# Performance work log

Measured on AMD Instinct MI355X. Metric: run time of the kernel, lower is better.

The kernel has to match this reference:

```python
import jax, jax.numpy as jnp
import numpy as np

T, B, F = 160, 640, 40          # time-major input [T, B, F]
H, PJ, L = 768, 256, 3          # nb_hidden, nb_proj, nb_layers
FORGET_BIAS = 1.0               # TF LSTMCell default


def _glorot(k, shape):
    std = (2.0 / (shape[0] + shape[1])) ** 0.5
    return jax.random.normal(k, shape, jnp.float32) * std


def setup_inputs() -> dict:
    key = jax.random.key(0)
    ks = jax.random.split(key, 7)
    x = jax.random.normal(ks[0], (T, B, F), jnp.float32)
    # layer 0: input dim F + proj state PJ; layers 1,2: input dim PJ + PJ
    W0 = _glorot(ks[1], (F + PJ, 4 * H)); b0 = jnp.zeros((4 * H,), jnp.float32)
    P0 = _glorot(ks[2], (H, PJ))
    W1 = _glorot(ks[3], (PJ + PJ, 4 * H)); b1 = jnp.zeros((4 * H,), jnp.float32)
    P1 = _glorot(ks[4], (H, PJ))
    W2 = _glorot(ks[5], (PJ + PJ, 4 * H)); b2 = jnp.zeros((4 * H,), jnp.float32)
    P2 = _glorot(ks[6], (H, PJ))
    return {"x": x, "W0": W0, "b0": b0, "P0": P0,
            "W1": W1, "b1": b1, "P1": P1,
            "W2": W2, "b2": b2, "P2": P2}


def _cell(xt, c, h, W, b, P):
    # TF LSTMCell with num_proj: gates on [x, m_prev]; gate order i, j, f, o.
    z = jnp.concatenate([xt, h], axis=-1) @ W + b            # [B, 4H]
    i, j, f, o = jnp.split(z, 4, axis=-1)
    c_new = jax.nn.sigmoid(f + FORGET_BIAS) * c + jax.nn.sigmoid(i) * jnp.tanh(j)
    m = jax.nn.sigmoid(o) * jnp.tanh(c_new)                  # [B, H]
    h_new = m @ P                                            # projected state [B, PJ]
    return c_new, h_new


def reference(x, W0, b0, P0, W1, b1, P1, W2, b2, P2):
    params = ((W0, b0, P0), (W1, b1, P1), (W2, b2, P2))
    Bd = x.shape[1]
    init = tuple((jnp.zeros((Bd, H), x.dtype), jnp.zeros((Bd, PJ), x.dtype))
                 for _ in range(L))

    def step(carry, xt):
        inp = xt
        new = []
        for (c, h), (W, b, P) in zip(carry, params):
            c, h = _cell(inp, c, h, W, b, P)
            new.append((c, h))
            inp = h
        return tuple(new), None

    carry, _ = jax.lax.scan(step, init, x)
    emb = carry[-1][1]                                       # last layer h at final step, [B, PJ]
    # tf.nn.l2_normalize
    return emb / jnp.sqrt(jnp.maximum(jnp.sum(emb * emb, axis=-1, keepdims=True), 1e-12))
```

## Files before the change

kernel.cpp:

```cpp
#include <hip/hip_runtime.h>

#define Bdim 640
#define Hdim 768
#define PJdim 256
#define Tdim 160
#define NSTEP (Tdim + 2)
#define ZS 258

typedef _Float16 half8 __attribute__((ext_vector_type(8)));
typedef float floatx4 __attribute__((ext_vector_type(4)));

constexpr size_t HB_HALFS = 3ull * Bdim * PJdim;
constexpr size_t ZP_OFF   = HB_HALFS * 2;
constexpr size_t MB_OFF   = ZP_OFF + 256;
constexpr size_t MB_HALFS = 3ull * Bdim * Hdim;
constexpr size_t X_OFF    = MB_OFF + MB_HALFS * 2;
constexpr size_t X_HALFS  = (size_t)Tdim * Bdim * 40;
constexpr size_t W_OFF    = X_OFF + X_HALFS * 2;
constexpr size_t W_HALFS  = 36ull * 131072;
constexpr size_t P_OFF    = W_OFF + W_HALFS * 2;
constexpr size_t P_HALFS  = 3ull * 196608;
constexpr size_t C_OFF    = P_OFF + P_HALFS * 2;
constexpr size_t C_BYTES  = 3ull * Bdim * Hdim * 4;

__device__ __forceinline__ float sigm(float v) { return 1.0f / (1.0f + __expf(-v)); }
__device__ __forceinline__ float tanh_fast(float v) { return 2.0f / (1.0f + __expf(-2.0f * v)) - 1.0f; }

__device__ __forceinline__ uint4 ld_coh16(const void* p) {
    const unsigned long long* q = (const unsigned long long*)p;
    unsigned long long a = __hip_atomic_load(q,     __ATOMIC_RELAXED, __HIP_MEMORY_SCOPE_AGENT);
    unsigned long long b = __hip_atomic_load(q + 1, __ATOMIC_RELAXED, __HIP_MEMORY_SCOPE_AGENT);
    uint4 r; r.x = (unsigned)a; r.y = (unsigned)(a >> 32);
    r.z = (unsigned)b; r.w = (unsigned)(b >> 32);
    return r;
}
__device__ __forceinline__ void st_coh16b(void* p, _Float16 h) {
    union { _Float16 h; unsigned short u; } cv; cv.h = h;
    __hip_atomic_store((unsigned short*)p, cv.u, __ATOMIC_RELAXED, __HIP_MEMORY_SCOPE_AGENT);
}

__device__ __forceinline__ void wait1(unsigned* c, unsigned tgt)
{
    if (threadIdx.x == 0) {
        while (__hip_atomic_load(c, __ATOMIC_RELAXED, __HIP_MEMORY_SCOPE_AGENT) < tgt)
            __builtin_amdgcn_s_sleep(1);
    }
    asm volatile("buffer_inv sc0" ::: "memory");
    __syncthreads();
}

__device__ __forceinline__ void wait2(unsigned* a, unsigned* b, unsigned tgt)
{
    if (threadIdx.x == 0) {
        while (__hip_atomic_load(a, __ATOMIC_RELAXED, __HIP_MEMORY_SCOPE_AGENT) < tgt)
            __builtin_amdgcn_s_sleep(1);
        while (__hip_atomic_load(b, __ATOMIC_RELAXED, __HIP_MEMORY_SCOPE_AGENT) < tgt)
            __builtin_amdgcn_s_sleep(1);
    }
    asm volatile("buffer_inv sc0" ::: "memory");
    __syncthreads();
}

__device__ __forceinline__ void pipe_sig(unsigned* c)
{
    __syncthreads();
    if (threadIdx.x == 0)
        __hip_atomic_fetch_add(c, 1u, __ATOMIC_RELAXED, __HIP_MEMORY_SCOPE_AGENT);
}

__device__ __forceinline__ void pipe_sig2(unsigned* a, unsigned* b)
{
    __syncthreads();
    if (threadIdx.x == 0) {
        __hip_atomic_fetch_add(a, 1u, __ATOMIC_RELAXED, __HIP_MEMORY_SCOPE_AGENT);
        __hip_atomic_fetch_add(b, 1u, __ATOMIC_RELAXED, __HIP_MEMORY_SCOPE_AGENT);
    }
}

__global__ void repack_kernel(const float* __restrict__ x,
                              const float* __restrict__ W0, const float* __restrict__ W1,
                              const float* __restrict__ W2, const float* __restrict__ P0,
                              const float* __restrict__ P1, const float* __restrict__ P2,
                              _Float16* __restrict__ Wfrag, _Float16* __restrict__ Pfrag,
                              _Float16* __restrict__ x16)
{
    size_t idx = (size_t)blockIdx.x * 256 + threadIdx.x;
    if (idx < W_HALFS) {
        int slab = (int)(idx >> 17);
        int l = slab / 12, ht = slab % 12;
        int r  = (int)(idx & 131071);
        int kc = r >> 13;
        int r2 = r & 8191;
        int g  = r2 >> 11;
        int cf = (r2 >> 9) & 3;
        int u  = r2 & 511;
        int lane = u >> 3, e = u & 7;
        int qd = lane >> 4, ln = lane & 15;
        int k   = kc * 32 + qd * 8 + e;
        int col = g * Hdim + ht * 64 + cf * 16 + ln;
        float v;
        if (l == 0)      v = (k < 296) ? W0[(size_t)k * 3072 + col] : 0.0f;
        else if (l == 1) v = W1[(size_t)k * 3072 + col];
        else             v = W2[(size_t)k * 3072 + col];
        Wfrag[idx] = (_Float16)v;
    } else if (idx < W_HALFS + P_HALFS) {
        size_t i = idx - W_HALFS;
        int l = (int)(i / 196608);
        int r = (int)(i % 196608);
        int cq = r / 49152;
        int r2 = r % 49152;
        int kc = r2 / 2048;
        int r3 = r2 & 2047;
        int cgr = r3 >> 9;
        int u  = r3 & 511;
        int lane = u >> 3, e = u & 7;
        int qd = lane >> 4, ln = lane & 15;
        int k  = kc * 32 + qd * 8 + e;
        int pj = cq * 64 + cgr * 16 + ln;
        const float* P = (l == 0) ? P0 : (l == 1) ? P1 : P2;
        Pfrag[i] = (_Float16)P[(size_t)k * PJdim + pj];
    } else if (idx < W_HALFS + P_HALFS + X_HALFS) {
        size_t i = idx - W_HALFS - P_HALFS;
        x16[i] = (_Float16)x[i];
    }
}

__device__ __forceinline__ void gate_step(
    int l, int b0r, int h0, int t, bool xl,
    const half8 (&Breg)[16][2], float (&c)[16],
    const _Float16* __restrict__ x16, const _Float16* __restrict__ h16,
    const _Float16* __restrict__ zerop, _Float16* __restrict__ mbuf,
    _Float16* __restrict__ Ast, float* __restrict__ zst, const float* __restrict__ bst,
    unsigned* pd, unsigned pdt, unsigned* pdlo, unsigned pdlot, int tid)
{
    const int wv = tid >> 6, lane = tid & 63, qd = lane >> 4, ln = lane & 15;
    const int g = wv >> 1, hh = wv & 1;
    const int qd8 = qd * 8;
    const int rowg = b0r + wv * 16 + ln;

    const _Float16* xt  = x16 + ((size_t)t * Bdim + rowg) * 40;
    const _Float16* h0b = h16 + (size_t)rowg * PJdim - 40;
    const _Float16* lob = (l > 0) ? h16 + ((size_t)(l - 1) * Bdim + rowg) * PJdim : nullptr;
    const _Float16* hib = h16 + ((size_t)l * Bdim + rowg) * PJdim - 256;

    auto srcp = [&](int kc) -> const _Float16* {
        int k = kc * 32 + qd8;
        if (l == 0) return (k < 40) ? xt + k : (k < 296) ? h0b + k : zerop;
        return (k < 256) ? lob + k : hib + k;
    };

    floatx4 acc[8][2];
    const floatx4 fz = {0.f, 0.f, 0.f, 0.f};
#pragma unroll
    for (int i = 0; i < 8; ++i) { acc[i][0] = fz; acc[i][1] = fz; }

    _Float16* Aw = Ast + wv * 512 + lane * 8;

    auto stage_gemm = [&](int kc0, int nkc, bool coh) {
        const int ncp = nkc >> 1;
        uint4 p0 = coh ? ld_coh16(srcp(kc0))     : *(const uint4*)srcp(kc0);
        uint4 p1 = coh ? ld_coh16(srcp(kc0 + 1)) : *(const uint4*)srcp(kc0 + 1);
#pragma unroll
        for (int cp = 0; cp < 5; ++cp) {
            if (cp < ncp) {
                const int s0 = (cp & 1) * 2;
                *(uint4*)(Aw + (size_t)s0 * 4096)       = p0;
                *(uint4*)(Aw + (size_t)(s0 + 1) * 4096) = p1;
                if (cp + 1 < ncp) {
                    p0 = coh ? ld_coh16(srcp(kc0 + 2 * cp + 2)) : *(const uint4*)srcp(kc0 + 2 * cp + 2);
                    p1 = coh ? ld_coh16(srcp(kc0 + 2 * cp + 3)) : *(const uint4*)srcp(kc0 + 2 * cp + 3);
                }
                __syncthreads();
#pragma unroll
                for (int j = 0; j < 2; ++j) {
                    const _Float16* Ab = Ast + (size_t)(s0 + j) * 4096;
                    const int kc = kc0 + 2 * cp + j;
#pragma unroll
                    for (int rf = 0; rf < 8; ++rf) {
                        half8 af = *(const half8*)(Ab + rf * 512 + lane * 8);
                        acc[rf][0] = __builtin_amdgcn_mfma_f32_16x16x32_f16(af, Breg[kc][0], acc[rf][0], 0, 0, 0);
                        acc[rf][1] = __builtin_amdgcn_mfma_f32_16x16x32_f16(af, Breg[kc][1], acc[rf][1], 0, 0, 0);
                    }
                }
            }
        }
    };

    if (pd) wait1(pd, pdt);
    if (l == 0) {
        stage_gemm(0, 10, false);
    } else {
        stage_gemm(8, 8, false);
        if (pdlo) wait1(pdlo, pdlot);
        stage_gemm(0, 8, xl);
    }
    __syncthreads();

#pragma unroll
    for (int rf = 0; rf < 8; ++rf)
#pragma unroll
        for (int cf = 0; cf < 2; ++cf)
#pragma unroll
            for (int r = 0; r < 4; ++r)
                zst[(size_t)(rf * 16 + qd * 4 + r) * ZS + g * 64 + hh * 32 + cf * 16 + ln]
                    = acc[rf][cf][r];
    __syncthreads();

    const int row = tid >> 2, c0 = (tid & 3) * 16;
    const float* zrow = zst + (size_t)row * ZS;
    union { _Float16 h[16]; uint4 v[2]; } pk;
#pragma unroll
    for (int q = 0; q < 4; ++q) {
        const int o = q * 4;
        float4 zi = *(const float4*)(zrow + c0 + o);
        float4 zj = *(const float4*)(zrow + 64 + c0 + o);
        float4 zf = *(const float4*)(zrow + 128 + c0 + o);
        float4 zo = *(const float4*)(zrow + 192 + c0 + o);
        float4 bi = *(const float4*)(bst + c0 + o);
        float4 bj = *(const float4*)(bst + 64 + c0 + o);
        float4 bf = *(const float4*)(bst + 128 + c0 + o);
        float4 bo = *(const float4*)(bst + 192 + c0 + o);
        float cn0 = sigm(zf.x + bf.x) * c[o + 0] + sigm(zi.x + bi.x) * tanh_fast(zj.x + bj.x);
        float cn1 = sigm(zf.y + bf.y) * c[o + 1] + sigm(zi.y + bi.y) * tanh_fast(zj.y + bj.y);
        float cn2 = sigm(zf.z + bf.z) * c[o + 2] + sigm(zi.z + bi.z) * tanh_fast(zj.z + bj.z);
        float cn3 = sigm(zf.w + bf.w) * c[o + 3] + sigm(zi.w + bi.w) * tanh_fast(zj.w + bj.w);
        c[o + 0] = cn0; c[o + 1] = cn1; c[o + 2] = cn2; c[o + 3] = cn3;
        pk.h[o + 0] = (_Float16)(sigm(zo.x + bo.x) * tanh_fast(cn0));
        pk.h[o + 1] = (_Float16)(sigm(zo.y + bo.y) * tanh_fast(cn1));
        pk.h[o + 2] = (_Float16)(sigm(zo.z + bo.z) * tanh_fast(cn2));
        pk.h[o + 3] = (_Float16)(sigm(zo.w + bo.w) * tanh_fast(cn3));
    }
    _Float16* mb = mbuf + ((size_t)l * Bdim + b0r + row) * Hdim + h0 + c0;
    *(uint4*)mb       = pk.v[0];
    *(uint4*)(mb + 8) = pk.v[1];
}

__device__ __forceinline__ void proj_step(
    int l, int b0r, int cq, const half8 (&Preg)[24],
    const _Float16* __restrict__ mbuf, _Float16* __restrict__ h16,
    _Float16* __restrict__ AstA, _Float16* __restrict__ AstB, int tid, bool xstore,
    unsigned* gdhb, unsigned tgt)
{
    const int wv = tid >> 6, lane = tid & 63, qd = lane >> 4, ln = lane & 15;
    const int rh = wv >> 2, cgi = wv & 3;
    const int rowg = b0r + wv * 16 + ln;
    const _Float16* mrow = mbuf + ((size_t)l * Bdim + rowg) * Hdim + qd * 8;
    _Float16* wA = AstA + wv * 512 + lane * 8;
    _Float16* wB = AstB + wv * 512 + lane * 8;

    floatx4 pacc[4];
    const floatx4 fz = {0.f, 0.f, 0.f, 0.f};
#pragma unroll
    for (int i = 0; i < 4; ++i) pacc[i] = fz;

    if (gdhb) wait2(gdhb + 0, gdhb + 16, tgt);
    uint4 p0 = *(const uint4*)(mrow);
    uint4 p1 = *(const uint4*)(mrow + 32);
    uint4 p2 = *(const uint4*)(mrow + 64);
    uint4 p3 = *(const uint4*)(mrow + 96);
#pragma unroll
    for (int ch = 0; ch < 6; ++ch) {
        _Float16* W = (ch & 1) ? wB : wA;
        const _Float16* R = (ch & 1) ? AstB : AstA;
        *(uint4*)(W)                      = p0;
        *(uint4*)(W + (size_t)1 * 4096)   = p1;
        *(uint4*)(W + (size_t)2 * 4096)   = p2;
        *(uint4*)(W + (size_t)3 * 4096)   = p3;
        if (ch < 5) {
            if (gdhb) wait2(gdhb + (size_t)(2 * ch + 2) * 16,
                            gdhb + (size_t)(2 * ch + 3) * 16, tgt);
            p0 = *(const uint4*)(mrow + (4 * ch + 4) * 32);
            p1 = *(const uint4*)(mrow + (4 * ch + 5) * 32);
            p2 = *(const uint4*)(mrow + (4 * ch + 6) * 32);
            p3 = *(const uint4*)(mrow + (4 * ch + 7) * 32);
        }
        __syncthreads();
#pragma unroll
        for (int kk = 0; kk < 4; ++kk) {
            const _Float16* Ab = R + (size_t)kk * 4096;
#pragma unroll
            for (int rfl = 0; rfl < 4; ++rfl) {
                half8 af = *(const half8*)(Ab + (rh * 4 + rfl) * 512 + lane * 8);
                pacc[rfl] = __builtin_amdgcn_mfma_f32_16x16x32_f16(af, Preg[ch * 4 + kk], pacc[rfl], 0, 0, 0);
            }
        }
    }

    if (xstore) {
#pragma unroll
        for (int rfl = 0; rfl < 4; ++rfl)
#pragma unroll
            for (int r = 0; r < 4; ++r) {
                int row = b0r + (rh * 4 + rfl) * 16 + qd * 4 + r;
                st_coh16b(h16 + ((size_t)l * Bdim + row) * PJdim + cq * 64 + cgi * 16 + ln,
                          (_Float16)pacc[rfl][r]);
            }
    } else {
#pragma unroll
        for (int rfl = 0; rfl < 4; ++rfl)
#pragma unroll
            for (int r = 0; r < 4; ++r) {
                int row = b0r + (rh * 4 + rfl) * 16 + qd * 4 + r;
                h16[((size_t)l * Bdim + row) * PJdim + cq * 64 + cgi * 16 + ln] = (_Float16)pacc[rfl][r];
            }
    }
}

__device__ __forceinline__ void load_Breg(const _Float16* __restrict__ Wfrag, int l, int ht,
                                          int wv, int lane, half8 (&Breg)[16][2])
{
    const int g = wv >> 1, hh = wv & 1;
    const _Float16* wslab = Wfrag + ((size_t)(l * 12 + ht)) * 131072;
#pragma unroll
    for (int kc = 0; kc < 16; ++kc)
#pragma unroll
        for (int cf = 0; cf < 2; ++cf)
            Breg[kc][cf] = *(const half8*)(wslab + kc * 8192 + g * 2048 + (hh * 2 + cf) * 512 + lane * 8);
}

__device__ __forceinline__ void load_Preg(const _Float16* __restrict__ Pfrag, int l, int cq,
                                          int wv, int lane, half8 (&Preg)[24])
{
    const int cgi = wv & 3;
    const _Float16* pslab = Pfrag + (size_t)l * 196608 + (size_t)cq * 49152;
#pragma unroll
    for (int kc = 0; kc < 24; ++kc)
        Preg[kc] = *(const half8*)(pslab + kc * 2048 + cgi * 512 + lane * 8);
}

__device__ __forceinline__ void load_bst(const float* __restrict__ bias, int h0, int tid,
                                         float* __restrict__ bst)
{
    if (tid < 256) {
        int gg = tid >> 6, u = tid & 63;
        bst[tid] = bias[gg * Hdim + h0 + u] + ((gg == 2) ? 1.0f : 0.0f);
    }
}

__device__ __forceinline__ void finalize_row(const _Float16* __restrict__ h16,
                                             float* __restrict__ out, int row, int lane)
{
    const _Float16* e = h16 + ((size_t)2 * Bdim + row) * PJdim + lane * 4;
    float v0 = (float)e[0], v1 = (float)e[1], v2 = (float)e[2], v3 = (float)e[3];
    float ss = v0 * v0 + v1 * v1 + v2 * v2 + v3 * v3;
#pragma unroll
    for (int o = 32; o > 0; o >>= 1) ss += __shfl_xor(ss, o, 64);
    float rs = rsqrtf(fmaxf(ss, 1e-12f));
    float4 o4; o4.x = v0 * rs; o4.y = v1 * rs; o4.z = v2 * rs; o4.w = v3 * rs;
    *(float4*)(out + (size_t)row * PJdim + lane * 4) = o4;
}

__global__ __launch_bounds__(512)
void lstm_persist(const _Float16* __restrict__ x16, const _Float16* __restrict__ Wfrag,
                  const _Float16* __restrict__ Pfrag,
                  const float* __restrict__ bias0, const float* __restrict__ bias1,
                  const float* __restrict__ bias2,
                  _Float16* __restrict__ h16, _Float16* __restrict__ mbuf,
                  const _Float16* __restrict__ zerop, float* __restrict__ out,
                  unsigned* __restrict__ flags)
{
    __shared__ __align__(16) char LDSRAW[133120];
    _Float16* Ast  = (_Float16*)LDSRAW;
    float*    zst  = (float*)LDSRAW;
    float*    bst  = (float*)(LDSRAW + 132096);

    const int tid = threadIdx.x, bid = blockIdx.x;
    const int wv = tid >> 6, lane = tid & 63;

    const int xcd = bid & 7, slot = bid >> 3;
    const int gid = xcd * 2 + (slot >> 4);
    const int rr  = slot & 15;
    if (gid >= 15) return;
    const int bt2 = gid / 3, l = gid % 3;
    const int b0r = bt2 * 128;

    unsigned* gbase = flags + (size_t)gid * 256;
    unsigned* gd = gbase;
    unsigned* pd = gbase + 8;

    if (rr < 12) {
        const int ht = rr, h0 = ht * 64;
        const bool xl = ((gid & 1) == 0) && (l > 0);
        unsigned* gdh_self = gbase + 16 + (size_t)ht * 16;
        half8 Breg[16][2];
        load_Breg(Wfrag, l, ht, wv, lane, Breg);
        load_bst((l == 0) ? bias0 : (l == 1) ? bias1 : bias2, h0, tid, bst);
        float c[16];
#pragma unroll
        for (int u = 0; u < 16; ++u) c[u] = 0.f;
        unsigned* pd_lo = (l > 0) ? flags + (size_t)(gid - 1) * 256 + 8 : nullptr;
        for (int t = 0; t < Tdim; ++t) {
            gate_step(l, b0r, h0, t, xl, Breg, c, x16, h16, zerop, mbuf,
                      Ast, zst, bst,
                      pd, 4u * (unsigned)t,
                      pd_lo, (l > 0) ? 4u * (unsigned)(t + 1) : 0u, tid);
            pipe_sig2(gd, gdh_self);
        }
        if (l == 2 && rr < 8) {
            wait1(pd, 4u * (unsigned)Tdim);
            int row0 = b0r + rr * 16 + wv * 2;
            finalize_row(h16, out, row0, lane);
            finalize_row(h16, out, row0 + 1, lane);
        }
    } else {
        const int cq = rr - 12;
        const bool xstore = ((gid & 1) == 1) && (gid + 1 < 15) && ((gid + 1) % 3 != 0);
        unsigned* gdhb = gbase + 16;
        half8 Preg[24];
        load_Preg(Pfrag, l, cq, wv, lane, Preg);
        unsigned* gd_hi = (l < 2) ? flags + (size_t)(gid + 1) * 256 : nullptr;
        for (int t = 0; t < Tdim; ++t) {
            if (gd_hi && t > 0) wait1(gd_hi, 12u * (unsigned)t);
            proj_step(l, b0r, cq, Preg, mbuf, h16,
                      Ast, (_Float16*)(LDSRAW + 32768), tid, xstore,
                      gdhb, (unsigned)(t + 1));
            pipe_sig(pd);
        }
    }
}

__global__ __launch_bounds__(512)
void gate_fb(const _Float16* __restrict__ x16, const _Float16* __restrict__ Wfrag,
             const float* __restrict__ bias0, const float* __restrict__ bias1,
             const float* __restrict__ bias2,
             _Float16* __restrict__ h16, _Float16* __restrict__ mbuf,
             const _Float16* __restrict__ zerop, float* __restrict__ cfb, int s)
{
    __shared__ __align__(16) char LDSRAW[133120];
    _Float16* Ast  = (_Float16*)LDSRAW;
    float*    zst  = (float*)LDSRAW;
    float*    bst  = (float*)(LDSRAW + 132096);
    const int tid = threadIdx.x, bid = blockIdx.x;
    const int ht = bid % 12, z = bid / 12, l = z % 3, bt2 = z / 3;
    const int t = s - l;
    if (t < 0 || t >= Tdim) return;
    const int wv = tid >> 6, lane = tid & 63;
    const int b0r = bt2 * 128, h0 = ht * 64;
    half8 Breg[16][2];
    load_Breg(Wfrag, l, ht, wv, lane, Breg);
    load_bst((l == 0) ? bias0 : (l == 1) ? bias1 : bias2, h0, tid, bst);
    __syncthreads();
    const int row = tid >> 2, c0 = (tid & 3) * 16;
    float c[16];
#pragma unroll
    for (int u = 0; u < 16; ++u)
        c[u] = cfb[((size_t)l * Bdim + b0r + row) * Hdim + h0 + c0 + u];
    gate_step(l, b0r, h0, t, false, Breg, c, x16, h16, zerop, mbuf, Ast, zst, bst,
              nullptr, 0u, nullptr, 0u, tid);
#pragma unroll
    for (int u = 0; u < 16; ++u)
        cfb[((size_t)l * Bdim + b0r + row) * Hdim + h0 + c0 + u] = c[u];
}

__global__ __launch_bounds__(512)
void proj_fb(const _Float16* __restrict__ Pfrag, const _Float16* __restrict__ mbuf,
             _Float16* __restrict__ h16, int s)
{
    __shared__ __align__(16) char LDSRAW[65536];
    const int tid = threadIdx.x, bid = blockIdx.x;
    const int cq = bid & 3, z = bid >> 2, l = z % 3, bt2 = z / 3;
    const int tp = s - l;
    if (tp < 0 || tp >= Tdim) return;
    const int wv = tid >> 6, lane = tid & 63;
    half8 Preg[24];
    load_Preg(Pfrag, l, cq, wv, lane, Preg);
    proj_step(l, bt2 * 128, cq, Preg, mbuf, h16,
              (_Float16*)LDSRAW, (_Float16*)(LDSRAW + 32768), tid, false,
              nullptr, 0u);
}

__global__ __launch_bounds__(512)
void fin_fb(const _Float16* __restrict__ h16, float* __restrict__ out)
{
    int row = blockIdx.x * 8 + (threadIdx.x >> 6);
    finalize_row(h16, out, row, threadIdx.x & 63);
}

extern "C" void kernel_launch(void* const* d_in, const int* in_sizes, int n_in,
                              void* d_out, int out_size, void* d_ws, size_t ws_size,
                              hipStream_t stream)
{
    (void)in_sizes; (void)n_in; (void)out_size; (void)ws_size;
    const float* x  = (const float*)d_in[0];
    const float* W0 = (const float*)d_in[1];
    const float* b0 = (const float*)d_in[2];
    const float* P0 = (const float*)d_in[3];
    const float* W1 = (const float*)d_in[4];
    const float* b1 = (const float*)d_in[5];
    const float* P1 = (const float*)d_in[6];
    const float* W2 = (const float*)d_in[7];
    const float* b2 = (const float*)d_in[8];
    const float* P2 = (const float*)d_in[9];

    char* ws = (char*)d_ws;
    _Float16* h16   = (_Float16*)(ws);
    _Float16* zerop = (_Float16*)(ws + ZP_OFF);
    _Float16* mbuf  = (_Float16*)(ws + MB_OFF);
    _Float16* x16   = (_Float16*)(ws + X_OFF);
    _Float16* Wfrag = (_Float16*)(ws + W_OFF);
    _Float16* Pfrag = (_Float16*)(ws + P_OFF);
    float*    cfb   = (float*)(ws + C_OFF);
    unsigned* flags = (unsigned*)(ws + C_OFF);
    float*    outp  = (float*)d_out;

    hipMemsetAsync(ws, 0, ZP_OFF + 256, stream);
    hipMemsetAsync(cfb, 0, C_BYTES, stream);

    {
        constexpr size_t total = W_HALFS + P_HALFS + X_HALFS;
        int grid = (int)((total + 255) / 256);
        repack_kernel<<<grid, 256, 0, stream>>>(x, W0, W1, W2, P0, P1, P2, Wfrag, Pfrag, x16);
    }

    int occ = 0;
    hipError_t oe = hipOccupancyMaxActiveBlocksPerMultiprocessor(&occ, lstm_persist, 512, 0);
    bool coop = (oe == hipSuccess && occ >= 1);
    if (coop) {
        void* args[] = { (void*)&x16, (void*)&Wfrag, (void*)&Pfrag,
                         (void*)&b0, (void*)&b1, (void*)&b2,
                         (void*)&h16, (void*)&mbuf, (void*)&zerop, (void*)&outp,
                         (void*)&flags };
        hipError_t le = hipLaunchCooperativeKernel((const void*)lstm_persist,
                                                   dim3(256), dim3(512), args, 0, stream);
        if (le != hipSuccess) { (void)hipGetLastError(); coop = false; }
    }
    if (!coop) {
        for (int s = 0; s < NSTEP; ++s) {
            gate_fb<<<180, 512, 0, stream>>>(x16, Wfrag, b0, b1, b2, h16, mbuf, zerop, cfb, s);
            proj_fb<<<60, 512, 0, stream>>>(Pfrag, mbuf, h16, s);
        }
        fin_fb<<<80, 512, 0, stream>>>(h16, outp);
    }
}
```

Before: 5.143 ms.

## Deepen global-to-LDS prefetch to two stages with triple-buffered LDS in gate and proj GEMMs

Both the gate GEMM staging loop and the projection step now keep two chunks of A-operand loads in flight, held in two register sets, instead of one. LDS goes from two buffers to three, rotating by modulo 3, so a write to the next slot cannot overwrite data still being read. In the projection path the dependency-flag wait for chunk ch+2 is issued earlier and replaces the barrier when flags are present. This aims to hide global-load and inter-block flag latency in the sequential recurrence. The costs are more registers, more LDS, and a possible race if the flag wait does not also synchronise the block.

```diff
diff --git a/kernel.cpp b/kernel.cpp
--- a/kernel.cpp
+++ b/kernel.cpp
@@ -158,17 +158,30 @@
 
     auto stage_gemm = [&](int kc0, int nkc, bool coh) {
         const int ncp = nkc >> 1;
-        uint4 p0 = coh ? ld_coh16(srcp(kc0))     : *(const uint4*)srcp(kc0);
-        uint4 p1 = coh ? ld_coh16(srcp(kc0 + 1)) : *(const uint4*)srcp(kc0 + 1);
+        uint4 pa0, pa1, pb0, pb1;
+        pa0 = coh ? ld_coh16(srcp(kc0))     : *(const uint4*)srcp(kc0);
+        pa1 = coh ? ld_coh16(srcp(kc0 + 1)) : *(const uint4*)srcp(kc0 + 1);
+        pb0 = coh ? ld_coh16(srcp(kc0 + 2)) : *(const uint4*)srcp(kc0 + 2);
+        pb1 = coh ? ld_coh16(srcp(kc0 + 3)) : *(const uint4*)srcp(kc0 + 3);
 #pragma unroll
         for (int cp = 0; cp < 5; ++cp) {
             if (cp < ncp) {
-                const int s0 = (cp & 1) * 2;
-                *(uint4*)(Aw + (size_t)s0 * 4096)       = p0;
-                *(uint4*)(Aw + (size_t)(s0 + 1) * 4096) = p1;
-                if (cp + 1 < ncp) {
-                    p0 = coh ? ld_coh16(srcp(kc0 + 2 * cp + 2)) : *(const uint4*)srcp(kc0 + 2 * cp + 2);
-                    p1 = coh ? ld_coh16(srcp(kc0 + 2 * cp + 3)) : *(const uint4*)srcp(kc0 + 2 * cp + 3);
+                const int s0 = (cp % 3) * 2;
+                _Float16* W0 = Aw + (size_t)s0 * 4096;
+                if ((cp & 1) == 0) {
+                    *(uint4*)W0          = pa0;
+                    *(uint4*)(W0 + 4096) = pa1;
+                    if (cp + 2 < ncp) {
+                        pa0 = coh ? ld_coh16(srcp(kc0 + 2 * cp + 4)) : *(const uint4*)srcp(kc0 + 2 * cp + 4);
+                        pa1 = coh ? ld_coh16(srcp(kc0 + 2 * cp + 5)) : *(const uint4*)srcp(kc0 + 2 * cp + 5);
+                    }
+                } else {
+                    *(uint4*)W0          = pb0;
+                    *(uint4*)(W0 + 4096) = pb1;
+                    if (cp + 2 < ncp) {
+                        pb0 = coh ? ld_coh16(srcp(kc0 + 2 * cp + 4)) : *(const uint4*)srcp(kc0 + 2 * cp + 4);
+                        pb1 = coh ? ld_coh16(srcp(kc0 + 2 * cp + 5)) : *(const uint4*)srcp(kc0 + 2 * cp + 5);
+                    }
                 }
                 __syncthreads();
 #pragma unroll
@@ -238,43 +251,52 @@
 __device__ __forceinline__ void proj_step(
     int l, int b0r, int cq, const half8 (&Preg)[24],
     const _Float16* __restrict__ mbuf, _Float16* __restrict__ h16,
-    _Float16* __restrict__ AstA, _Float16* __restrict__ AstB, int tid, bool xstore,
+    _Float16* __restrict__ AstBase, int tid, bool xstore,
     unsigned* gdhb, unsigned tgt)
 {
     const int wv = tid >> 6, lane = tid & 63, qd = lane >> 4, ln = lane & 15;
     const int rh = wv >> 2, cgi = wv & 3;
     const int rowg = b0r + wv * 16 + ln;
     const _Float16* mrow = mbuf + ((size_t)l * Bdim + rowg) * Hdim + qd * 8;
-    _Float16* wA = AstA + wv * 512 + lane * 8;
-    _Float16* wB = AstB + wv * 512 + lane * 8;
 
     floatx4 pacc[4];
     const floatx4 fz = {0.f, 0.f, 0.f, 0.f};
 #pragma unroll
     for (int i = 0; i < 4; ++i) pacc[i] = fz;
 
+    uint4 pa[4], pb[4];
     if (gdhb) wait2(gdhb + 0, gdhb + 16, tgt);
-    uint4 p0 = *(const uint4*)(mrow);
-    uint4 p1 = *(const uint4*)(mrow + 32);
-    uint4 p2 = *(const uint4*)(mrow + 64);
-    uint4 p3 = *(const uint4*)(mrow + 96);
+#pragma unroll
+    for (int k = 0; k < 4; ++k) pa[k] = *(const uint4*)(mrow + k * 32);
+    if (gdhb) wait2(gdhb + 32, gdhb + 48, tgt);
+#pragma unroll
+    for (int k = 0; k < 4; ++k) pb[k] = *(const uint4*)(mrow + (4 + k) * 32);
+
 #pragma unroll
     for (int ch = 0; ch < 6; ++ch) {
-        _Float16* W = (ch & 1) ? wB : wA;
-        const _Float16* R = (ch & 1) ? AstB : AstA;
-        *(uint4*)(W)                      = p0;
-        *(uint4*)(W + (size_t)1 * 4096)   = p1;
-        *(uint4*)(W + (size_t)2 * 4096)   = p2;
-        *(uint4*)(W + (size_t)3 * 4096)   = p3;
-        if (ch < 5) {
-            if (gdhb) wait2(gdhb + (size_t)(2 * ch + 2) * 16,
-                            gdhb + (size_t)(2 * ch + 3) * 16, tgt);
-            p0 = *(const uint4*)(mrow + (4 * ch + 4) * 32);
-            p1 = *(const uint4*)(mrow + (4 * ch + 5) * 32);
-            p2 = *(const uint4*)(mrow + (4 * ch + 6) * 32);
-            p3 = *(const uint4*)(mrow + (4 * ch + 7) * 32);
-        }
-        __syncthreads();
+        _Float16* W = AstBase + (size_t)(ch % 3) * 16384 + wv * 512 + lane * 8;
+        const _Float16* R = AstBase + (size_t)(ch % 3) * 16384;
+        if ((ch & 1) == 0) {
+#pragma unroll
+            for (int k = 0; k < 4; ++k) *(uint4*)(W + (size_t)k * 4096) = pa[k];
+        } else {
+#pragma unroll
+            for (int k = 0; k < 4; ++k) *(uint4*)(W + (size_t)k * 4096) = pb[k];
+        }
+        if (ch + 2 < 6) {
+            if (gdhb) wait2(gdhb + (size_t)(2 * (ch + 2)) * 16,
+                            gdhb + (size_t)(2 * (ch + 2) + 1) * 16, tgt);
+            else __syncthreads();
+            if ((ch & 1) == 0) {
+#pragma unroll
+                for (int k = 0; k < 4; ++k) pa[k] = *(const uint4*)(mrow + ((ch + 2) * 4 + k) * 32);
+            } else {
+#pragma unroll
+                for (int k = 0; k < 4; ++k) pb[k] = *(const uint4*)(mrow + ((ch + 2) * 4 + k) * 32);
+            }
+        } else {
+            __syncthreads();
+        }
 #pragma unroll
         for (int kk = 0; kk < 4; ++kk) {
             const _Float16* Ab = R + (size_t)kk * 4096;
@@ -412,8 +434,7 @@
         for (int t = 0; t < Tdim; ++t) {
             if (gd_hi && t > 0) wait1(gd_hi, 12u * (unsigned)t);
             proj_step(l, b0r, cq, Preg, mbuf, h16,
-                      Ast, (_Float16*)(LDSRAW + 32768), tid, xstore,
-                      gdhb, (unsigned)(t + 1));
+                      Ast, tid, xstore, gdhb, (unsigned)(t + 1));
             pipe_sig(pd);
         }
     }
@@ -456,7 +477,7 @@
 void proj_fb(const _Float16* __restrict__ Pfrag, const _Float16* __restrict__ mbuf,
              _Float16* __restrict__ h16, int s)
 {
-    __shared__ __align__(16) char LDSRAW[65536];
+    __shared__ __align__(16) char LDSRAW[98304];
     const int tid = threadIdx.x, bid = blockIdx.x;
     const int cq = bid & 3, z = bid >> 2, l = z % 3, bt2 = z / 3;
     const int tp = s - l;
@@ -465,8 +486,7 @@
     half8 Preg[24];
     load_Preg(Pfrag, l, cq, wv, lane, Preg);
     proj_step(l, bt2 * 128, cq, Preg, mbuf, h16,
-              (_Float16*)LDSRAW, (_Float16*)(LDSRAW + 32768), tid, false,
-              nullptr, 0u);
+              (_Float16*)LDSRAW, tid, false, nullptr, 0u);
 }
 
 __global__ __launch_bounds__(512)
```

Result: slower. 6.392 ms (+24.3%).
